# Optimization experiments

Hardware: AMD Instinct MI355X
Metric: run time of the kernel (lower is better)

Reference implementation:

```python
import jax, jax.numpy as jnp
import numpy as np

DECAY = 0.999
EPS = 1e-5
COMMIT = 0.25
ORTHO_W = 10.0
NUM_ORTHO = 128


def setup_inputs() -> dict:
    key = jax.random.key(0)
    k1, k2 = jax.random.split(key)
    M, D = 2048, 512
    B, T = 32, 1024
    x = jax.random.normal(k1, (B, T, D), dtype=jnp.float32)
    init_bound = 1.0 / M
    emb = jax.random.uniform(k2, (M, D), minval=-init_bound, maxval=init_bound, dtype=jnp.float32)
    return {
        "x": x,
        "embedding": emb,
        "ema_count": jnp.zeros((M,), jnp.float32),
        "ema_weight": emb,  # torch init: ema_weight = embedding.clone()
    }


def reference(x, embedding, ema_count, ema_weight):
    M, D = embedding.shape
    x_sg = jax.lax.stop_gradient(x)
    x_flat = x_sg.reshape(-1, D)  # [N, D]

    distances = (jnp.sum(embedding * embedding, axis=1)[None, :]
                 + jnp.sum(x_flat * x_flat, axis=1, keepdims=True)
                 - 2.0 * (x_flat @ embedding.T))
    indices = jnp.argmin(distances.astype(jnp.float32), axis=-1)  # [N]

    quantized = embedding[indices].reshape(x.shape)

    # EMA updates (training=True). one_hot(indices).sum(0) == scatter-add counts;
    # encodings.T @ x_flat == scatter-add of x rows into code slots.
    counts = jnp.zeros((M,), x.dtype).at[indices].add(1.0)
    new_count = DECAY * ema_count + (1.0 - DECAY) * counts
    n = jnp.sum(new_count)
    new_count = (new_count + EPS) / (n + M * EPS) * n
    dw = jnp.zeros((M, D), x.dtype).at[indices].add(x_flat)
    new_weight = DECAY * ema_weight + (1.0 - DECAY) * dw
    new_embedding = new_weight / new_count[:, None]

    codebook_loss = jnp.mean((x_sg - quantized) ** 2)
    e_latent_loss = jnp.mean((x - jax.lax.stop_gradient(quantized)) ** 2)
    commitment_loss = COMMIT * e_latent_loss

    quant_st = x + jax.lax.stop_gradient(quantized - x)  # straight-through

    # ortho loss over used codes of the UPDATED codebook (torch: self.embedding post-EMA).
    # Deterministic jit-safe variant of unique+randperm: take the first NUM_ORTHO
    # used code ids (stable argsort puts used codes first), mask padding if fewer.
    used = counts > 0
    order = jnp.argsort(jnp.where(used, 0, 1).astype(jnp.int32))  # stable sort
    sel = order[:NUM_ORTHO]
    valid = used[sel].astype(x.dtype)  # [NUM_ORTHO]
    codebk = new_embedding[sel]
    norm = jnp.maximum(jnp.linalg.norm(codebk, axis=-1, keepdims=True), 1e-12)
    normed = (codebk / norm) * valid[:, None]
    cosine_sim = normed @ normed.T
    n_valid = jnp.sum(valid)
    ortho_loss = jnp.sum((cosine_sim - jnp.diag(valid)) ** 2) / (n_valid * n_valid) * ORTHO_W

    return (quant_st, commitment_loss, codebook_loss, ortho_loss, indices,
            new_embedding, new_count, new_weight)
```

## Files before the change

kernel.cpp:

```cpp
#include <hip/hip_runtime.h>
#include <math.h>

#define N_ROWS 32768
#define M_CODES 2048
#define D_DIM 512
#define MARGIN 1.2e-3f
#define CAND_CAP 32

#define OUT_QST       0
#define OUT_COMMIT    16777216
#define OUT_CODEBOOK  16777217
#define OUT_ORTHO     16777218
#define OUT_INDICES   16777219
#define OUT_NEWEMB    16809987
#define OUT_NEWCOUNT  17858563
#define OUT_NEWW      17860611

#define WS_COUNTS     0
#define WS_CURSOR     2048
#define WS_SSE        4096
#define WS_ORTHO      4097
#define WS_CANDCNT    4104
#define WS_ZERO_FLOATS 36872
#define WS_E2         36872
#define WS_X2         38920
#define WS_IDX        71688
#define WS_NCN        104456
#define WS_SEL        106504
#define WS_VALID      106632
#define WS_NVALID     106760
#define WS_NORMED     106768
#define WS_NORMEDT    172304
#define WS_OFFS       237840
#define WS_ORDER      239896
#define WS_CANDC      272664
#define WS_CANDD      1321240
#define WS_XH         2369816
#define WS_EH         10758424
#define WS_TOTAL_FLOATS 11282712

typedef __attribute__((ext_vector_type(8))) short short8v;
typedef __attribute__((ext_vector_type(4))) float f32x4;

__device__ __forceinline__ unsigned short f2bf(float f) {
    unsigned u = __float_as_uint(f);
    unsigned r = (u + 0x7fffu + ((u >> 16) & 1u)) >> 16;
    return (unsigned short)r;
}
__device__ __forceinline__ int fkey(float f) {
    int b = __float_as_int(f);
    return b >= 0 ? b : (b ^ 0x7fffffff);
}
__device__ __forceinline__ float kinv(int k) {
    int b = k >= 0 ? k : (k ^ 0x7fffffff);
    return __int_as_float(b);
}

#define GLOAD16(g, s) __builtin_amdgcn_global_load_lds( \
    (const __attribute__((address_space(1))) void*)(g), \
    (__attribute__((address_space(3))) void*)(s), 16, 0, 0)

__global__ __launch_bounds__(256) void prep_kernel(const float* __restrict__ emb,
                                                   const float* __restrict__ x,
                                                   float* __restrict__ e2,
                                                   float* __restrict__ x2,
                                                   unsigned short* __restrict__ xh,
                                                   unsigned short* __restrict__ eh) {
    int row  = blockIdx.x * 4 + (threadIdx.x >> 6);
    int lane = threadIdx.x & 63;
    bool is_e = row < M_CODES;
    const float* src = is_e ? (emb + (size_t)row * D_DIM)
                            : (x + (size_t)(row - M_CODES) * D_DIM);
    unsigned short* dh = is_e ? (eh + (size_t)row * D_DIM)
                              : (xh + (size_t)(row - M_CODES) * D_DIM);
    float4 a = *(const float4*)(src + lane * 4);
    float4 b = *(const float4*)(src + 256 + lane * 4);
    float s = a.x*a.x + a.y*a.y + a.z*a.z + a.w*a.w
            + b.x*b.x + b.y*b.y + b.z*b.z + b.w*b.w;
#pragma unroll
    for (int o = 32; o > 0; o >>= 1) s += __shfl_xor(s, o, 64);

    ushort4 h0, h1;
    h0.x = f2bf(a.x); h0.y = f2bf(a.y); h0.z = f2bf(a.z); h0.w = f2bf(a.w);
    h1.x = f2bf(b.x); h1.y = f2bf(b.y); h1.z = f2bf(b.z); h1.w = f2bf(b.w);
    *(ushort4*)(dh + lane * 4)       = h0;
    *(ushort4*)(dh + 256 + lane * 4) = h1;

    if (lane == 0) {
        if (is_e) e2[row] = s;
        else      x2[row - M_CODES] = s;
    }
}

__global__ __launch_bounds__(256) void sq_kernel(const float* __restrict__ emb,
                                                 const float* __restrict__ x,
                                                 float* __restrict__ e2,
                                                 float* __restrict__ x2) {
    int row  = blockIdx.x * 4 + (threadIdx.x >> 6);
    int lane = threadIdx.x & 63;
    const float* src = (row < M_CODES) ? (emb + (size_t)row * D_DIM)
                                       : (x + (size_t)(row - M_CODES) * D_DIM);
    float4 a = *(const float4*)(src + lane * 4);
    float4 b = *(const float4*)(src + 256 + lane * 4);
    float s = a.x*a.x + a.y*a.y + a.z*a.z + a.w*a.w
            + b.x*b.x + b.y*b.y + b.z*b.z + b.w*b.w;
#pragma unroll
    for (int o = 32; o > 0; o >>= 1) s += __shfl_xor(s, o, 64);
    if (lane == 0) {
        if (row < M_CODES) e2[row] = s;
        else               x2[row - M_CODES] = s;
    }
}

__global__ __launch_bounds__(256) void approx_kernel(const unsigned short* __restrict__ xh,
                                                     const unsigned short* __restrict__ eh,
                                                     const float* __restrict__ e2g,
                                                     int* __restrict__ candcnt,
                                                     int* __restrict__ candC,
                                                     float* __restrict__ candD) {
    __shared__ short Ah[128 * 64], Bh[128 * 64];
    __shared__ int rowminI[128];

    const int t = threadIdx.x;
    const int w = t >> 6;
    const int l = t & 63;
    const int ml = l & 15;
    const int q  = l >> 4;
    const int rw = (w & 1) * 64;
    const int cw = (w >> 1) * 64;

    const int bid = blockIdx.x;
    const int row_tile = (bid >> 5) * 8 + (bid & 7);
    const int sub = (bid >> 3) & 3;
    const int row0 = row_tile * 128;
    const int code_base = sub * 512;

    if (t < 128) rowminI[t] = 0x7fffffff;

    const int grow = l >> 3;
    const int pg8  = (((l & 7) ^ grow)) * 8;

    for (int ct = 0; ct < 4; ++ct) {
        const int code0 = code_base + ct * 128;

        f32x4 acc[4][4];
#pragma unroll
        for (int mi = 0; mi < 4; ++mi)
#pragma unroll
            for (int ni = 0; ni < 4; ++ni) acc[mi][ni] = (f32x4)0.f;

        for (int k0 = 0; k0 < D_DIM; k0 += 64) {
            __syncthreads();
#pragma unroll
            for (int i = 0; i < 4; ++i) {
                int r = i * 32 + w * 8 + grow;
                GLOAD16(xh + (size_t)(row0 + r) * D_DIM + k0 + pg8, &Ah[i * 2048 + w * 512]);
                GLOAD16(eh + (size_t)(code0 + r) * D_DIM + k0 + pg8, &Bh[i * 2048 + w * 512]);
            }
            __syncthreads();

#pragma unroll
            for (int kk = 0; kk < 64; kk += 32) {
                const int pbase = kk >> 3;
                short8v a[4];
#pragma unroll
                for (int mi = 0; mi < 4; ++mi) {
                    int m = rw + mi * 16 + ml;
                    a[mi] = *(const short8v*)(&Ah[m * 64 + ((((pbase + q) ^ (m & 7))) << 3)]);
                }
#pragma unroll
                for (int ni = 0; ni < 4; ++ni) {
                    int n = cw + ni * 16 + ml;
                    short8v b = *(const short8v*)(&Bh[n * 64 + ((((pbase + q) ^ (n & 7))) << 3)]);
#pragma unroll
                    for (int mi = 0; mi < 4; ++mi)
                        acc[mi][ni] = __builtin_amdgcn_mfma_f32_16x16x32_bf16(a[mi], b, acc[mi][ni], 0, 0, 0);
                }
            }
        }

        float e2v[4];
#pragma unroll
        for (int ni = 0; ni < 4; ++ni) e2v[ni] = e2g[code0 + cw + ni * 16 + ml];

#pragma unroll
        for (int mi = 0; mi < 4; ++mi)
#pragma unroll
            for (int ni = 0; ni < 4; ++ni)
#pragma unroll
                for (int r = 0; r < 4; ++r)
                    acc[mi][ni][r] = e2v[ni] - 2.0f * acc[mi][ni][r];

#pragma unroll
        for (int mi = 0; mi < 4; ++mi)
#pragma unroll
            for (int r = 0; r < 4; ++r) {
                float v = fminf(fminf(acc[mi][0][r], acc[mi][1][r]),
                                fminf(acc[mi][2][r], acc[mi][3][r]));
#pragma unroll
                for (int o = 1; o < 16; o <<= 1) v = fminf(v, __shfl_xor(v, o, 64));
                if (ml == 0) atomicMin(&rowminI[rw + mi * 16 + q * 4 + r], fkey(v));
            }
        __syncthreads();

#pragma unroll
        for (int mi = 0; mi < 4; ++mi)
#pragma unroll
            for (int r = 0; r < 4; ++r) {
                int row_l = rw + mi * 16 + q * 4 + r;
                float rm = kinv(rowminI[row_l]);
                int row_g = row0 + row_l;
#pragma unroll
                for (int ni = 0; ni < 4; ++ni) {
                    float d = acc[mi][ni][r];
                    if (d <= rm + MARGIN) {
                        int pos = atomicAdd(&candcnt[row_g], 1);
                        if (pos < CAND_CAP) {
                            candC[row_g * CAND_CAP + pos] = code0 + cw + ni * 16 + ml;
                            candD[row_g * CAND_CAP + pos] = d;
                        }
                    }
                }
            }
    }
}

__global__ __launch_bounds__(256) void rerank_qst_kernel(const float* __restrict__ x,
                                                         const float* __restrict__ emb,
                                                         const float* __restrict__ e2,
                                                         const float* __restrict__ x2,
                                                         const int* __restrict__ candcnt,
                                                         const int* __restrict__ candC,
                                                         const float* __restrict__ candD,
                                                         float* __restrict__ counts,
                                                         int* __restrict__ idx_out,
                                                         float* __restrict__ idxf_out,
                                                         float* __restrict__ sse,
                                                         float* __restrict__ qst) {
    __shared__ float ssered[4];
    const int w = threadIdx.x >> 6;
    const int lane = threadIdx.x & 63;
    const int row = blockIdx.x * 4 + w;

    int cnt = candcnt[row];
    int best_c;

    if (cnt > CAND_CAP) {
        const float x2r = x2[row];
        const float* xr = x + (size_t)row * D_DIM;
        float bd = 3.0e38f;
        int   bc = 0x7fffffff;
        for (int c = lane; c < M_CODES; c += 64) {
            const float* er = emb + (size_t)c * D_DIM;
            float dot = 0.f;
            for (int k = 0; k < D_DIM; ++k) dot = fmaf(xr[k], er[k], dot);
            float d = (x2r + e2[c]) - 2.0f * dot;
            if (d < bd || (d == bd && c < bc)) { bd = d; bc = c; }
        }
#pragma unroll
        for (int o = 32; o > 0; o >>= 1) {
            float od = __shfl_xor(bd, o, 64);
            int   oc = __shfl_xor(bc, o, 64);
            if (od < bd || (od == bd && oc < bc)) { bd = od; bc = oc; }
        }
        best_c = bc;
    } else {
        float d = 3.0e38f;
        int   c = 0x7fffffff;
        if (lane < cnt) {
            d = candD[row * CAND_CAP + lane];
            c = candC[row * CAND_CAP + lane];
        }
        float dmin = d;
#pragma unroll
        for (int o = 32; o > 0; o >>= 1) dmin = fminf(dmin, __shfl_xor(dmin, o, 64));

        bool surv = (lane < cnt) && (d <= dmin + MARGIN);
        unsigned long long mask = __ballot(surv);

        if (__popcll(mask) == 1) {
            int src = __ffsll((long long)mask) - 1;
            best_c = __shfl(c, src, 64);
        } else {
            const float x2r = x2[row];
            const float* xr = x + (size_t)row * D_DIM;
            float4 xa = *(const float4*)(xr + lane * 8);
            float4 xb = *(const float4*)(xr + lane * 8 + 4);
            float bd = 3.0e38f;
            int   bc = 0x7fffffff;
            unsigned long long m = mask;
            while (m) {
                int src = __ffsll((long long)m) - 1;
                m &= m - 1;
                int cs = __shfl(c, src, 64);
                const float* er = emb + (size_t)cs * D_DIM;
                float4 ea = *(const float4*)(er + lane * 8);
                float4 eb = *(const float4*)(er + lane * 8 + 4);
                float dot = xa.x*ea.x + xa.y*ea.y + xa.z*ea.z + xa.w*ea.w
                          + xb.x*eb.x + xb.y*eb.y + xb.z*eb.z + xb.w*eb.w;
#pragma unroll
                for (int o = 32; o > 0; o >>= 1) dot += __shfl_xor(dot, o, 64);
                float t1 = x2r + e2[cs];
                float dex = t1 - 2.0f * dot;
                if (dex < bd || (dex == bd && cs < bc)) { bd = dex; bc = cs; }
            }
            best_c = bc;
        }
    }

    {
        const float* xr = x + (size_t)row * D_DIM;
        const float* er = emb + (size_t)best_c * D_DIM;
        float loss = 0.f;
#pragma unroll
        for (int j = 0; j < 2; ++j) {
            const int off = j * 256 + lane * 4;
            float4 xv = *(const float4*)(xr + off);
            float4 qv = *(const float4*)(er + off);
            float4 qs;
            qs.x = xv.x + (qv.x - xv.x);
            qs.y = xv.y + (qv.y - xv.y);
            qs.z = xv.z + (qv.z - xv.z);
            qs.w = xv.w + (qv.w - xv.w);
            *(float4*)(qst + (size_t)row * D_DIM + off) = qs;
            float dx;
            dx = xv.x - qv.x; loss += dx * dx;
            dx = xv.y - qv.y; loss += dx * dx;
            dx = xv.z - qv.z; loss += dx * dx;
            dx = xv.w - qv.w; loss += dx * dx;
        }
#pragma unroll
        for (int o = 32; o > 0; o >>= 1) loss += __shfl_xor(loss, o, 64);

        if (lane == 0) {
            idx_out[row] = best_c;
            idxf_out[row] = (float)best_c;
            atomicAdd(&counts[best_c], 1.0f);
            ssered[w] = loss;
        }
    }
    __syncthreads();
    if (threadIdx.x == 0)
        atomicAdd(sse, ssered[0] + ssered[1] + ssered[2] + ssered[3]);
}

__global__ __launch_bounds__(256) void argmin_kernel(const float* __restrict__ x,
                                                     const float* __restrict__ emb,
                                                     const float* __restrict__ e2,
                                                     const float* __restrict__ x2,
                                                     int* __restrict__ idx_out,
                                                     float* __restrict__ idxf_out) {
    __shared__ float As[64][36];
    __shared__ float Bs[32][68];
    __shared__ float e2s[64];
    __shared__ float redD[64][17];
    __shared__ int   redI[64][17];

    const int t  = threadIdx.x;
    const int tx = t & 15;
    const int ty = t >> 4;
    const int row0 = blockIdx.x * 64;

    float rmin[4];
    int   ridx[4];
#pragma unroll
    for (int r = 0; r < 4; ++r) { rmin[r] = 3.0e38f; ridx[r] = 0; }

    float x2r[4];
#pragma unroll
    for (int r = 0; r < 4; ++r) x2r[r] = x2[row0 + ty * 4 + r];

    const int lr = t >> 3;
    const int lc = t & 7;

    for (int m0 = 0; m0 < M_CODES; m0 += 64) {
        __syncthreads();
        if (t < 64) e2s[t] = e2[m0 + t];

        float acc[4][4];
#pragma unroll
        for (int r = 0; r < 4; ++r)
#pragma unroll
            for (int c = 0; c < 4; ++c) acc[r][c] = 0.f;

        for (int k0 = 0; k0 < D_DIM; k0 += 32) {
            __syncthreads();
#pragma unroll
            for (int p = 0; p < 2; ++p) {
                int r = p * 32 + lr;
                float4 v = *(const float4*)(x + (size_t)(row0 + r) * D_DIM + k0 + lc * 4);
                *(float4*)(&As[r][lc * 4]) = v;
            }
#pragma unroll
            for (int p = 0; p < 2; ++p) {
                int r = p * 32 + lr;
                float4 v = *(const float4*)(emb + (size_t)(m0 + r) * D_DIM + k0 + lc * 4);
                Bs[lc * 4 + 0][r] = v.x;
                Bs[lc * 4 + 1][r] = v.y;
                Bs[lc * 4 + 2][r] = v.z;
                Bs[lc * 4 + 3][r] = v.w;
            }
            __syncthreads();

#pragma unroll
            for (int kk = 0; kk < 32; kk += 4) {
                float av[4][4], bv[4][4];
#pragma unroll
                for (int r = 0; r < 4; ++r) {
                    float4 a4 = *(const float4*)(&As[ty * 4 + r][kk]);
                    av[r][0] = a4.x; av[r][1] = a4.y; av[r][2] = a4.z; av[r][3] = a4.w;
                }
#pragma unroll
                for (int j = 0; j < 4; ++j) {
                    float4 b4 = *(const float4*)(&Bs[kk + j][tx * 4]);
                    bv[j][0] = b4.x; bv[j][1] = b4.y; bv[j][2] = b4.z; bv[j][3] = b4.w;
                }
#pragma unroll
                for (int j = 0; j < 4; ++j)
#pragma unroll
                    for (int r = 0; r < 4; ++r)
#pragma unroll
                        for (int c = 0; c < 4; ++c)
                            acc[r][c] += av[r][j] * bv[j][c];
            }
        }

#pragma unroll
        for (int c = 0; c < 4; ++c) {
            int mm = tx * 4 + c;
            int m  = m0 + mm;
            float e2v = e2s[mm];
#pragma unroll
            for (int r = 0; r < 4; ++r) {
                float t1 = x2r[r] + e2v;
                float dd  = t1 - 2.0f * acc[r][c];
                if (dd < rmin[r]) { rmin[r] = dd; ridx[r] = m; }
            }
        }
    }

    __syncthreads();
#pragma unroll
    for (int r = 0; r < 4; ++r) {
        redD[ty * 4 + r][tx] = rmin[r];
        redI[ty * 4 + r][tx] = ridx[r];
    }
    __syncthreads();
    if (t < 64) {
        float best = redD[t][0];
        int   bi   = redI[t][0];
#pragma unroll
        for (int i = 1; i < 16; ++i) {
            float dd = redD[t][i];
            int   ii = redI[t][i];
            if (dd < best || (dd == best && ii < bi)) { best = dd; bi = ii; }
        }
        idx_out[row0 + t]  = bi;
        idxf_out[row0 + t] = (float)bi;
    }
}

__global__ __launch_bounds__(256) void hist_kernel(const int* __restrict__ idx,
                                                   float* __restrict__ counts) {
    int r = blockIdx.x * 256 + threadIdx.x;
    atomicAdd(&counts[idx[r]], 1.0f);
}

__global__ __launch_bounds__(256) void qst_sse_kernel(const float* __restrict__ x,
                                                      const float* __restrict__ emb,
                                                      const int* __restrict__ idx,
                                                      float* __restrict__ sse,
                                                      float* __restrict__ qst) {
    const int w    = threadIdx.x >> 6;
    const int lane = threadIdx.x & 63;
    const int rowbase = blockIdx.x * 16 + w * 4;
    float loss = 0.f;
    for (int i = 0; i < 4; ++i) {
        const int row = rowbase + i;
        const int m   = idx[row];
#pragma unroll
        for (int j = 0; j < 2; ++j) {
            const int off = j * 256 + lane * 4;
            float4 xv = *(const float4*)(x + (size_t)row * D_DIM + off);
            float4 qv = *(const float4*)(emb + (size_t)m * D_DIM + off);
            float4 qs;
            qs.x = xv.x + (qv.x - xv.x);
            qs.y = xv.y + (qv.y - xv.y);
            qs.z = xv.z + (qv.z - xv.z);
            qs.w = xv.w + (qv.w - xv.w);
            *(float4*)(qst + (size_t)row * D_DIM + off) = qs;
            float dx;
            dx = xv.x - qv.x; loss += dx * dx;
            dx = xv.y - qv.y; loss += dx * dx;
            dx = xv.z - qv.z; loss += dx * dx;
            dx = xv.w - qv.w; loss += dx * dx;
        }
    }
#pragma unroll
    for (int o = 32; o > 0; o >>= 1) loss += __shfl_xor(loss, o, 64);
    if (lane == 0) atomicAdd(sse, loss);
}

__global__ __launch_bounds__(256) void f1scan_kernel(const float* __restrict__ ema_count,
                                                     const float* __restrict__ counts,
                                                     float* __restrict__ out_newcount,
                                                     float* __restrict__ nc_ws,
                                                     int* __restrict__ offs) {
    __shared__ float red[256];
    __shared__ int pre[257];
    int t = threadIdx.x;
    float raw[8];
    int   c[8];
    float part = 0.f;
    int   s = 0;
#pragma unroll
    for (int i = 0; i < 8; ++i) {
        int m = t * 8 + i;
        float cm = counts[m];
        raw[i] = 0.999f * ema_count[m] + 0.001f * cm;
        part += raw[i];
        c[i] = (int)cm;
        s += c[i];
    }
    red[t] = part;
    pre[t] = s;
    __syncthreads();
    for (int st = 128; st > 0; st >>= 1) {
        if (t < st) red[t] += red[t + st];
        __syncthreads();
    }
    if (t == 0) {
        int run = 0;
        for (int i = 0; i < 256; ++i) { int v = pre[i]; pre[i] = run; run += v; }
        pre[256] = run;
    }
    __syncthreads();
    float n = red[0];
    float denom = n + (float)M_CODES * 1e-5f;
    int base = pre[t];
#pragma unroll
    for (int i = 0; i < 8; ++i) {
        int m = t * 8 + i;
        float v = (raw[i] + 1e-5f) / denom * n;
        out_newcount[m] = v;
        nc_ws[m] = v;
        offs[m] = base; base += c[i];
    }
}

__global__ __launch_bounds__(256) void fill_kernel(const int* __restrict__ idx,
                                                   const int* __restrict__ offs,
                                                   int* __restrict__ cursor,
                                                   int* __restrict__ order) {
    int r = blockIdx.x * 256 + threadIdx.x;
    int m = idx[r];
    int pos = atomicAdd(&cursor[m], 1);
    order[offs[m] + pos] = r;
}

__global__ __launch_bounds__(256) void gather_nw_kernel(const float* __restrict__ x,
                                                        const float* __restrict__ ema_weight,
                                                        const float* __restrict__ ncn,
                                                        const float* __restrict__ counts,
                                                        const int* __restrict__ offs,
                                                        const int* __restrict__ order,
                                                        float* __restrict__ out_ne,
                                                        float* __restrict__ out_nw) {
    const int m = blockIdx.x;
    const int t = threadIdx.x;
    const int beg = offs[m];
    const int end = beg + (int)counts[m];
    float ax = 0.f, ay = 0.f;
    for (int j = beg; j < end; ++j) {
        int r = order[j];
        float2 v = *(const float2*)(x + (size_t)r * D_DIM + t * 2);
        ax += v.x; ay += v.y;
    }
    size_t i = (size_t)m * D_DIM + t * 2;
    float2 wv = *(const float2*)(ema_weight + i);
    float  c  = ncn[m];
    float2 nw, ne;
    nw.x = 0.999f * wv.x + 0.001f * ax; ne.x = nw.x / c;
    nw.y = 0.999f * wv.y + 0.001f * ay; ne.y = nw.y / c;
    *(float2*)(out_nw + i) = nw;
    *(float2*)(out_ne + i) = ne;
}

__global__ __launch_bounds__(256) void g1_kernel(const float* __restrict__ counts,
                                                 const float* __restrict__ new_emb,
                                                 int* __restrict__ sel,
                                                 float* __restrict__ valid,
                                                 float* __restrict__ n_valid,
                                                 float* __restrict__ normed,
                                                 float* __restrict__ normedT) {
    __shared__ int pre[257];
    int t = threadIdx.x;
    int u = 0;
#pragma unroll
    for (int i = 0; i < 8; ++i) u += (counts[t * 8 + i] > 0.f) ? 1 : 0;
    pre[t] = u;
    __syncthreads();
    if (t == 0) {
        int run = 0;
        for (int i = 0; i < 256; ++i) { int c = pre[i]; pre[i] = run; run += c; }
        pre[256] = run;
    }
    __syncthreads();
    int U = pre[256];
    int base = pre[t];
    int run = 0;
    for (int i = 0; i < 8; ++i) {
        int m = t * 8 + i;
        bool used = counts[m] > 0.f;
        int ur = base + run;
        if (used) {
            if (ur < 128) sel[ur] = m;
            run++;
        } else {
            int pos = U + (m - ur);
            if (pos < 128) sel[pos] = m;
        }
    }
    __syncthreads();
    if (t < 128) valid[t] = (counts[sel[t]] > 0.f) ? 1.f : 0.f;
    __syncthreads();
    if (t == 0) {
        float s = 0.f;
        for (int i = 0; i < 128; ++i) s += valid[i];
        *n_valid = s;
    }
    int w = t >> 6, lane = t & 63;
    for (int r = w; r < 128; r += 4) {
        int sm = sel[r];
        const float* src = new_emb + (size_t)sm * D_DIM;
        float4 a = *(const float4*)(src + lane * 4);
        float4 b = *(const float4*)(src + 256 + lane * 4);
        float s = a.x*a.x + a.y*a.y + a.z*a.z + a.w*a.w
                + b.x*b.x + b.y*b.y + b.z*b.z + b.w*b.w;
#pragma unroll
        for (int o = 32; o > 0; o >>= 1) s += __shfl_xor(s, o, 64);
        float norm = fmaxf(sqrtf(s), 1e-12f);
        float vv = valid[r];
        float4 na, nb;
        na.x = a.x / norm * vv; na.y = a.y / norm * vv;
        na.z = a.z / norm * vv; na.w = a.w / norm * vv;
        nb.x = b.x / norm * vv; nb.y = b.y / norm * vv;
        nb.z = b.z / norm * vv; nb.w = b.w / norm * vv;
        *(float4*)(normed + (size_t)r * D_DIM + lane * 4) = na;
        *(float4*)(normed + (size_t)r * D_DIM + 256 + lane * 4) = nb;
        normedT[(lane * 4 + 0) * 128 + r] = na.x;
        normedT[(lane * 4 + 1) * 128 + r] = na.y;
        normedT[(lane * 4 + 2) * 128 + r] = na.z;
        normedT[(lane * 4 + 3) * 128 + r] = na.w;
        normedT[(256 + lane * 4 + 0) * 128 + r] = nb.x;
        normedT[(256 + lane * 4 + 1) * 128 + r] = nb.y;
        normedT[(256 + lane * 4 + 2) * 128 + r] = nb.z;
        normedT[(256 + lane * 4 + 3) * 128 + r] = nb.w;
    }
}

__global__ __launch_bounds__(128) void g2_kernel(const float* __restrict__ normed,
                                                 const float* __restrict__ normedT,
                                                 const float* __restrict__ valid,
                                                 float* __restrict__ ortho_acc) {
    __shared__ float rowi[512];
    __shared__ float red[128];
    int i = blockIdx.x, t = threadIdx.x;
    *(float4*)(rowi + t * 4) = *(const float4*)(normed + (size_t)i * D_DIM + t * 4);
    __syncthreads();
    float dot = 0.f;
    for (int k = 0; k < D_DIM; ++k) dot += rowi[k] * normedT[k * 128 + t];
    float diag = (i == t) ? valid[i] : 0.f;
    float d = dot - diag;
    red[t] = d * d;
    __syncthreads();
    for (int s = 64; s > 0; s >>= 1) {
        if (t < s) red[t] += red[t + s];
        __syncthreads();
    }
    if (t == 0) atomicAdd(ortho_acc, red[0]);
}

__global__ void g3_kernel(const float* __restrict__ sse,
                          const float* __restrict__ ortho_acc,
                          const float* __restrict__ n_valid,
                          float* __restrict__ out3) {
    if (threadIdx.x == 0 && blockIdx.x == 0) {
        float m = *sse / 16777216.f;
        out3[0] = 0.25f * m;
        out3[1] = m;
        float nv = *n_valid;
        out3[2] = *ortho_acc / (nv * nv) * 10.f;
    }
}

extern "C" void kernel_launch(void* const* d_in, const int* in_sizes, int n_in,
                              void* d_out, int out_size, void* d_ws, size_t ws_size,
                              hipStream_t stream) {
    const float* x          = (const float*)d_in[0];
    const float* emb        = (const float*)d_in[1];
    const float* ema_count  = (const float*)d_in[2];
    const float* ema_weight = (const float*)d_in[3];
    float* out = (float*)d_out;
    float* ws  = (float*)d_ws;

    float* counts  = ws + WS_COUNTS;
    int*   cursor  = (int*)(ws + WS_CURSOR);
    float* sse     = ws + WS_SSE;
    float* ortho   = ws + WS_ORTHO;
    int*   candcnt = (int*)(ws + WS_CANDCNT);
    float* e2      = ws + WS_E2;
    float* x2      = ws + WS_X2;
    int*   idxws   = (int*)(ws + WS_IDX);
    float* ncn     = ws + WS_NCN;
    int*   sel     = (int*)(ws + WS_SEL);
    float* valid   = ws + WS_VALID;
    float* nvalid  = ws + WS_NVALID;
    float* normed  = ws + WS_NORMED;
    float* normedT = ws + WS_NORMEDT;
    int*   offs    = (int*)(ws + WS_OFFS);
    int*   order   = (int*)(ws + WS_ORDER);
    int*   candC   = (int*)(ws + WS_CANDC);
    float* candD   = ws + WS_CANDD;
    unsigned short* xh = (unsigned short*)(ws + WS_XH);
    unsigned short* eh = (unsigned short*)(ws + WS_EH);

    const bool big_ws = ws_size >= (size_t)WS_TOTAL_FLOATS * sizeof(float);

    hipMemsetAsync(ws, 0, (size_t)WS_ZERO_FLOATS * sizeof(float), stream);

    if (big_ws) {
        prep_kernel<<<(M_CODES + N_ROWS) / 4, 256, 0, stream>>>(emb, x, e2, x2, xh, eh);
        approx_kernel<<<1024, 256, 0, stream>>>(xh, eh, e2, candcnt, candC, candD);
        rerank_qst_kernel<<<N_ROWS / 4, 256, 0, stream>>>(x, emb, e2, x2, candcnt, candC,
                                                          candD, counts, idxws,
                                                          out + OUT_INDICES, sse,
                                                          out + OUT_QST);
    } else {
        sq_kernel<<<(M_CODES + N_ROWS) / 4, 256, 0, stream>>>(emb, x, e2, x2);
        argmin_kernel<<<N_ROWS / 64, 256, 0, stream>>>(x, emb, e2, x2, idxws,
                                                       out + OUT_INDICES);
        hist_kernel<<<N_ROWS / 256, 256, 0, stream>>>(idxws, counts);
        qst_sse_kernel<<<N_ROWS / 16, 256, 0, stream>>>(x, emb, idxws, sse, out + OUT_QST);
    }

    f1scan_kernel<<<1, 256, 0, stream>>>(ema_count, counts, out + OUT_NEWCOUNT, ncn, offs);

    fill_kernel<<<N_ROWS / 256, 256, 0, stream>>>(idxws, offs, cursor, order);

    gather_nw_kernel<<<M_CODES, 256, 0, stream>>>(x, ema_weight, ncn, counts, offs, order,
                                                  out + OUT_NEWEMB, out + OUT_NEWW);

    g1_kernel<<<1, 256, 0, stream>>>(counts, out + OUT_NEWEMB, sel, valid, nvalid,
                                     normed, normedT);

    g2_kernel<<<128, 128, 0, stream>>>(normed, normedT, valid, ortho);

    g3_kernel<<<1, 64, 0, stream>>>(sse, ortho, nvalid, out + OUT_COMMIT);
}
```

Measured before the change: 541.5 us.

## Double-buffer LDS tiles in approx kernel with async prefetch across code tiles

New measurement: 654.9 us. 1.21x slower.

```diff
diff --git a/kernel.cpp b/kernel.cpp
--- a/kernel.cpp
+++ b/kernel.cpp
@@ -112,13 +112,13 @@
     }
 }
 
-__global__ __launch_bounds__(256) void approx_kernel(const unsigned short* __restrict__ xh,
-                                                     const unsigned short* __restrict__ eh,
-                                                     const float* __restrict__ e2g,
-                                                     int* __restrict__ candcnt,
-                                                     int* __restrict__ candC,
-                                                     float* __restrict__ candD) {
-    __shared__ short Ah[128 * 64], Bh[128 * 64];
+__global__ __launch_bounds__(256) void approx7_kernel(const unsigned short* __restrict__ xh,
+                                                      const unsigned short* __restrict__ eh,
+                                                      const float* __restrict__ e2g,
+                                                      int* __restrict__ candcnt,
+                                                      int* __restrict__ candC,
+                                                      float* __restrict__ candD) {
+    __shared__ short Ah[2][8192], Bh[2][8192];
     __shared__ int rowminI[128];
 
     const int t = threadIdx.x;
@@ -140,25 +140,49 @@
     const int grow = l >> 3;
     const int pg8  = (((l & 7) ^ grow)) * 8;
 
+#define STAGE7(bufv, sv) do {                                                       \
+    const int ct_ = (sv) >> 3;                                                      \
+    const int k0_ = ((sv) & 7) * 64;                                                \
+    const int cb_ = code_base + ct_ * 128;                                          \
+    _Pragma("unroll")                                                               \
+    for (int i_ = 0; i_ < 4; ++i_) {                                                \
+        int r_ = i_ * 32 + w * 8 + grow;                                            \
+        GLOAD16(xh + (size_t)(row0 + r_) * D_DIM + k0_ + pg8,                       \
+                &Ah[(bufv)][i_ * 2048 + w * 512]);                                  \
+        GLOAD16(eh + (size_t)(cb_ + r_) * D_DIM + k0_ + pg8,                        \
+                &Bh[(bufv)][i_ * 2048 + w * 512]);                                  \
+    }                                                                               \
+} while (0)
+
+    __syncthreads();
+
+    STAGE7(0, 0);
+    STAGE7(1, 1);
+
     for (int ct = 0; ct < 4; ++ct) {
         const int code0 = code_base + ct * 128;
 
+        float e2v[4];
+#pragma unroll
+        for (int ni = 0; ni < 4; ++ni) e2v[ni] = e2g[code0 + cw + ni * 16 + ml];
+
         f32x4 acc[4][4];
 #pragma unroll
         for (int mi = 0; mi < 4; ++mi)
 #pragma unroll
             for (int ni = 0; ni < 4; ++ni) acc[mi][ni] = (f32x4)0.f;
 
-        for (int k0 = 0; k0 < D_DIM; k0 += 64) {
-            __syncthreads();
-#pragma unroll
-            for (int i = 0; i < 4; ++i) {
-                int r = i * 32 + w * 8 + grow;
-                GLOAD16(xh + (size_t)(row0 + r) * D_DIM + k0 + pg8, &Ah[i * 2048 + w * 512]);
-                GLOAD16(eh + (size_t)(code0 + r) * D_DIM + k0 + pg8, &Bh[i * 2048 + w * 512]);
-            }
-            __syncthreads();
-
+        for (int k0s = 0; k0s < 8; ++k0s) {
+            const int s = ct * 8 + k0s;
+
+            if (s < 31) asm volatile("s_waitcnt vmcnt(8)" ::: "memory");
+            else        asm volatile("s_waitcnt vmcnt(0)" ::: "memory");
+            __builtin_amdgcn_s_barrier();
+            asm volatile("" ::: "memory");
+
+            const int cur = s & 1;
+            const short* Ab = &Ah[cur][0];
+            const short* Bb = &Bh[cur][0];
 #pragma unroll
             for (int kk = 0; kk < 64; kk += 32) {
                 const int pbase = kk >> 3;
@@ -166,22 +190,24 @@
 #pragma unroll
                 for (int mi = 0; mi < 4; ++mi) {
                     int m = rw + mi * 16 + ml;
-                    a[mi] = *(const short8v*)(&Ah[m * 64 + ((((pbase + q) ^ (m & 7))) << 3)]);
+                    a[mi] = *(const short8v*)(&Ab[m * 64 + ((((pbase + q) ^ (m & 7))) << 3)]);
                 }
 #pragma unroll
                 for (int ni = 0; ni < 4; ++ni) {
                     int n = cw + ni * 16 + ml;
-                    short8v b = *(const short8v*)(&Bh[n * 64 + ((((pbase + q) ^ (n & 7))) << 3)]);
+                    short8v b = *(const short8v*)(&Bb[n * 64 + ((((pbase + q) ^ (n & 7))) << 3)]);
 #pragma unroll
                     for (int mi = 0; mi < 4; ++mi)
                         acc[mi][ni] = __builtin_amdgcn_mfma_f32_16x16x32_bf16(a[mi], b, acc[mi][ni], 0, 0, 0);
                 }
             }
-        }
-
-        float e2v[4];
-#pragma unroll
-        for (int ni = 0; ni < 4; ++ni) e2v[ni] = e2g[code0 + cw + ni * 16 + ml];
+
+            asm volatile("s_waitcnt lgkmcnt(0)" ::: "memory");
+            __builtin_amdgcn_s_barrier();
+            asm volatile("" ::: "memory");
+
+            if (s < 30) STAGE7(cur, s + 2);
+        }
 
 #pragma unroll
         for (int mi = 0; mi < 4; ++mi)
@@ -201,7 +227,9 @@
                 for (int o = 1; o < 16; o <<= 1) v = fminf(v, __shfl_xor(v, o, 64));
                 if (ml == 0) atomicMin(&rowminI[rw + mi * 16 + q * 4 + r], fkey(v));
             }
-        __syncthreads();
+        asm volatile("s_waitcnt lgkmcnt(0)" ::: "memory");
+        __builtin_amdgcn_s_barrier();
+        asm volatile("" ::: "memory");
 
 #pragma unroll
         for (int mi = 0; mi < 4; ++mi)
@@ -223,6 +251,7 @@
                 }
             }
     }
+#undef STAGE7
 }
 
 __global__ __launch_bounds__(256) void rerank_qst_kernel(const float* __restrict__ x,
@@ -731,7 +760,7 @@
 
     if (big_ws) {
         prep_kernel<<<(M_CODES + N_ROWS) / 4, 256, 0, stream>>>(emb, x, e2, x2, xh, eh);
-        approx_kernel<<<1024, 256, 0, stream>>>(xh, eh, e2, candcnt, candC, candD);
+        approx7_kernel<<<1024, 256, 0, stream>>>(xh, eh, e2, candcnt, candC, candD);
         rerank_qst_kernel<<<N_ROWS / 4, 256, 0, stream>>>(x, emb, e2, x2, candcnt, candC,
                                                           candD, counts, idxws,
                                                           out + OUT_INDICES, sse,
```
